# Kernel tuning notes

Hardware: AMD Instinct MI355X
Metric: run time of the kernel (lower is better)

The kernel has to match this reference:

```python
import jax, jax.numpy as jnp
import numpy as np

N_WIN = 232
T = 8
KERNEL = (2, 2, 2)
STRIDE = (2, 2, 2)
SLOPE = 25.0  # fast_sigmoid surrogate slope


@jax.custom_vjp
def spike(v):
    # heaviside(v) with fast-sigmoid surrogate gradient
    return (v > 0).astype(v.dtype)

def _spike_fwd(v):
    return spike(v), v

def _spike_bwd(v, g):
    return (g / (SLOPE * jnp.abs(v) + 1.0) ** 2,)

spike.defvjp(_spike_fwd, _spike_bwd)


def _avg_pool3d(x, kernel, stride):
    # x: (B, C, D, H, W), VALID pooling
    win = (1, 1) + tuple(kernel)
    st = (1, 1) + tuple(stride)
    s = jax.lax.reduce_window(x, 0.0, jax.lax.add, win, st, 'VALID')
    return s / float(np.prod(kernel))


def setup_inputs() -> dict:
    key = jax.random.key(0)
    ks = jax.random.split(key, 14)
    B, C, H, W = 64, 3, 32, 32
    input_dim, h0, h1, n_cls = 256, 256, 128, 6
    x = jax.random.normal(ks[0], (B, C, N_WIN, H, W), jnp.float32)
    W_in = jax.random.normal(ks[1], (h0, input_dim), jnp.float32) * 0.05
    b_in = jnp.zeros((h0,), jnp.float32)
    W_hid = jax.random.normal(ks[2], (h1, h0), jnp.float32) * 0.05
    b_hid = jnp.zeros((h1,), jnp.float32)
    in_feat = C * h1 * 14  # C * hidden[1] * D'
    W_out = jax.random.normal(ks[3], (n_cls, in_feat), jnp.float32) * 0.05
    b_out = jnp.zeros((n_cls,), jnp.float32)
    beta_in = jax.random.uniform(ks[4], (h0,), jnp.float32)
    thr_in = jax.random.uniform(ks[5], (h0,), jnp.float32)
    beta_hid = jax.random.uniform(ks[6], (h1,), jnp.float32)
    thr_hid = jax.random.uniform(ks[7], (h1,), jnp.float32)
    beta_out = jax.random.uniform(ks[8], (n_cls,), jnp.float32)
    return dict(x=x, W_in=W_in, b_in=b_in, W_hid=W_hid, b_hid=b_hid,
                W_out=W_out, b_out=b_out, beta_in=beta_in, thr_in=thr_in,
                beta_hid=beta_hid, thr_hid=thr_hid, beta_out=beta_out)


def _lif(mem, cur, beta, thr):
    # snntorch Leaky, reset-by-subtract; reset uses detached prev-mem spike
    reset = jax.lax.stop_gradient((mem > thr).astype(mem.dtype))
    mem = jnp.clip(beta, 0.0, 1.0) * mem + cur - reset * thr
    spk = spike(mem - thr)
    return spk, mem


def reference(x, W_in, b_in, W_hid, b_hid, W_out, b_out,
              beta_in, thr_in, beta_hid, thr_hid, beta_out):
    B, C, _, H, W = x.shape
    chunk = N_WIN // T  # 29
    # split depth into T chunks: (T, B, C, chunk, H, W)
    xt = x.reshape(B, C, T, chunk, H, W).transpose(2, 0, 1, 3, 4, 5)
    pooled = jax.vmap(lambda v: _avg_pool3d(v, KERNEL, STRIDE))(xt)  # (T,B,C,D',H',W')
    _, _, _, Dp, Hp, Wp = pooled.shape
    pr = pooled.reshape(T, B, C * Dp, Hp * Wp)
    # fc_in applied to all timesteps at once (recurrence-free)
    cur_in_all = jnp.einsum('tbnf,hf->tbnh', pr, W_in) + b_in  # (T,B,N,h0)

    h0 = W_in.shape[0]
    h1 = W_hid.shape[0]
    n_cls = W_out.shape[0]
    N = C * Dp
    mem_in0 = jnp.zeros((B, N, h0), x.dtype)
    mem_hid0 = jnp.zeros((B, N, h1), x.dtype)
    mem_out0 = jnp.zeros((B, n_cls), x.dtype)

    def step(carry, cur_in):
        mem_in, mem_hid, mem_out = carry
        spk_in, mem_in = _lif(mem_in, cur_in, beta_in, thr_in)
        cur_hid = jnp.einsum('bnh,gh->bng', spk_in, W_hid) + b_hid
        spk_hid, mem_hid = _lif(mem_hid, cur_hid, beta_hid, thr_hid)
        flat = spk_hid.reshape(spk_hid.shape[0], -1)  # (B, N*h1)
        cur_out = flat @ W_out.T + b_out
        spk_out, mem_out = _lif(mem_out, cur_out, beta_out, jnp.float32(1.0))
        return (mem_in, mem_hid, mem_out), spk_out

    _, spk_rec = jax.lax.scan(step, (mem_in0, mem_hid0, mem_out0), cur_in_all)
    return spk_rec  # (T, B, n_classes)
```

## Files before the change

kernel.cpp:

```cpp
#include <hip/hip_runtime.h>

#define T_STEPS 8
#define NROW    42
#define BN      2688
#define H0      256
#define H1      128
#define KFLAT   5376


#define SWA(r)  ((r) + ((r) >> 5) * 4)

__global__ __launch_bounds__(256, 3) void snn_front(
        const float* __restrict__ x,
        const float* __restrict__ Wi,
        const float* __restrict__ bi,
        const float* __restrict__ beti,
        const float* __restrict__ thri,
        const float* __restrict__ Wh,
        const float* __restrict__ bh,
        const float* __restrict__ beth,
        const float* __restrict__ thrh,
        float* __restrict__ spkh) {
    __shared__ float smem[9216 + 2240];
    float* S   = smem;
    float* At  = smem;
    float* Bt  = smem + 576;
    float* Bt2 = smem + 9216;

    int tid = threadIdx.x;
    int gbase = blockIdx.x * 4;

    int wp = tid & 15;
    int q  = tid >> 4;
    const float* xb0;
    const float* xb1;
    int mloc0 = q * 2, mloc1 = q * 2 + 1;
    {
        int g = gbase + (mloc0 >> 3);
        int t = mloc0 & 7;
        int b = g / 42, r = g - b * 42;
        int c = r / 14, dp = r - c * 14;
        xb0 = x + ((long)b * 712704 + (long)c * 237568
                + (long)(t * 29 + 2 * dp) * 1024 + 2 * wp);
    }
    {
        int g = gbase + (mloc1 >> 3);
        int t = mloc1 & 7;
        int b = g / 42, r = g - b * 42;
        int c = r / 14, dp = r - c * 14;
        xb1 = x + ((long)b * 712704 + (long)c * 237568
                + (long)(t * 29 + 2 * dp) * 1024 + 2 * wp);
    }

    const float* Bp = Wi + (long)tid * 256;
    int bcol = SWA(tid);

    int tm = tid & 3;
    int tn = tid >> 2;
    int ca = tm * 8;
    int cb = SWA(tn * 4);

    float acc[8][4] = {};

    for (int k0 = 0; k0 < 256; k0 += 16) {
        int hp = k0 >> 4;
        const float* p0 = xb0 + hp * 64;
        const float* p1 = xb1 + hp * 64;
        float2 a00 = *(const float2*)(p0);
        float2 a01 = *(const float2*)(p0 + 32);
        float2 a02 = *(const float2*)(p0 + 1024);
        float2 a03 = *(const float2*)(p0 + 1056);
        float2 a10 = *(const float2*)(p1);
        float2 a11 = *(const float2*)(p1 + 32);
        float2 a12 = *(const float2*)(p1 + 1024);
        float2 a13 = *(const float2*)(p1 + 1056);
        float4 w0 = *(const float4*)(Bp + k0);
        float4 w1 = *(const float4*)(Bp + k0 + 4);
        float4 w2 = *(const float4*)(Bp + k0 + 8);
        float4 w3 = *(const float4*)(Bp + k0 + 12);
        __syncthreads();
        float s0 = a00.x + a00.y + a01.x + a01.y + a02.x + a02.y + a03.x + a03.y;
        float s1 = a10.x + a10.y + a11.x + a11.y + a12.x + a12.y + a13.x + a13.y;
        At[wp * 36 + mloc0] = s0 * 0.125f;
        At[wp * 36 + mloc1] = s1 * 0.125f;
        Bt[ 0 * 284 + bcol] = w0.x; Bt[ 1 * 284 + bcol] = w0.y;
        Bt[ 2 * 284 + bcol] = w0.z; Bt[ 3 * 284 + bcol] = w0.w;
        Bt[ 4 * 284 + bcol] = w1.x; Bt[ 5 * 284 + bcol] = w1.y;
        Bt[ 6 * 284 + bcol] = w1.z; Bt[ 7 * 284 + bcol] = w1.w;
        Bt[ 8 * 284 + bcol] = w2.x; Bt[ 9 * 284 + bcol] = w2.y;
        Bt[10 * 284 + bcol] = w2.z; Bt[11 * 284 + bcol] = w2.w;
        Bt[12 * 284 + bcol] = w3.x; Bt[13 * 284 + bcol] = w3.y;
        Bt[14 * 284 + bcol] = w3.z; Bt[15 * 284 + bcol] = w3.w;
        __syncthreads();
#pragma unroll
        for (int k = 0; k < 16; ++k) {
            float4 av0 = *(const float4*)&At[k * 36 + ca];
            float4 av1 = *(const float4*)&At[k * 36 + ca + 4];
            float4 bv  = *(const float4*)&Bt[k * 284 + cb];
            float am[8] = {av0.x, av0.y, av0.z, av0.w, av1.x, av1.y, av1.z, av1.w};
            float bb[4] = {bv.x, bv.y, bv.z, bv.w};
#pragma unroll
            for (int i = 0; i < 8; ++i)
#pragma unroll
                for (int j = 0; j < 4; ++j)
                    acc[i][j] = fmaf(am[i], bb[j], acc[i][j]);
        }
    }

#pragma unroll
    for (int j = 0; j < 4; ++j) {
        int h = tn * 4 + j;
        float be = fminf(fmaxf(beti[h], 0.f), 1.f);
        float th = thri[h];
        float bb = bi[h];
        float mem = 0.f;
#pragma unroll
        for (int t = 0; t < T_STEPS; ++t) {
            float cur = acc[t][j] + bb;
            float reset = (mem > th) ? th : 0.f;
            mem = be * mem + cur - reset;
            acc[t][j] = ((mem - th) > 0.f) ? 1.f : 0.f;
        }
    }

    __syncthreads();
#pragma unroll
    for (int j = 0; j < 4; ++j) {
        int h = tn * 4 + j;
#pragma unroll
        for (int t = 0; t < T_STEPS; ++t)
            S[h * 36 + ca + t] = acc[t][j];
    }

    const float* Bp2 = Wh + (long)(tid >> 1) * 256 + (tid & 1) * 8;
    int bcol2 = SWA(tid >> 1);
    int cb2 = SWA(tn * 2);
    float acc2[8][2] = {};

    for (int k0 = 0; k0 < 256; k0 += 16) {
        float4 u0 = *(const float4*)(Bp2 + k0);
        float4 u1 = *(const float4*)(Bp2 + k0 + 4);
        __syncthreads();
        int kb = (tid & 1) * 8;
        Bt2[(kb + 0) * 140 + bcol2] = u0.x; Bt2[(kb + 1) * 140 + bcol2] = u0.y;
        Bt2[(kb + 2) * 140 + bcol2] = u0.z; Bt2[(kb + 3) * 140 + bcol2] = u0.w;
        Bt2[(kb + 4) * 140 + bcol2] = u1.x; Bt2[(kb + 5) * 140 + bcol2] = u1.y;
        Bt2[(kb + 6) * 140 + bcol2] = u1.z; Bt2[(kb + 7) * 140 + bcol2] = u1.w;
        __syncthreads();
#pragma unroll
        for (int k = 0; k < 16; ++k) {
            float4 av0 = *(const float4*)&S[(k0 + k) * 36 + ca];
            float4 av1 = *(const float4*)&S[(k0 + k) * 36 + ca + 4];
            float2 bv  = *(const float2*)&Bt2[k * 140 + cb2];
            float am[8] = {av0.x, av0.y, av0.z, av0.w, av1.x, av1.y, av1.z, av1.w};
#pragma unroll
            for (int i = 0; i < 8; ++i) {
                acc2[i][0] = fmaf(am[i], bv.x, acc2[i][0]);
                acc2[i][1] = fmaf(am[i], bv.y, acc2[i][1]);
            }
        }
    }

#pragma unroll
    for (int j = 0; j < 2; ++j) {
        int h = tn * 2 + j;
        float be = fminf(fmaxf(beth[h], 0.f), 1.f);
        float th = thrh[h];
        float bb = bh[h];
        float mem = 0.f;
#pragma unroll
        for (int t = 0; t < T_STEPS; ++t) {
            float cur = acc2[t][j] + bb;
            float reset = (mem > th) ? th : 0.f;
            mem = be * mem + cur - reset;
            acc2[t][j] = ((mem - th) > 0.f) ? 1.f : 0.f;
        }
    }
    int rbase = blockIdx.x * 32 + tm * 8;
#pragma unroll
    for (int t = 0; t < T_STEPS; ++t) {
        float2 o = {acc2[t][0], acc2[t][1]};
        *(float2*)&spkh[(long)(rbase + t) * 128 + tn * 2] = o;
    }
}

__global__ __launch_bounds__(256) void out_gemm(const float* __restrict__ spkh,
                                                const float* __restrict__ W_out,
                                                const float* __restrict__ b_out,
                                                float* __restrict__ cur_out) {
    __shared__ float part[256][8];
    int row = blockIdx.x;
    int t = row >> 6, b = row & 63;
    int tid = threadIdx.x;
    float acc[6] = {0.f, 0.f, 0.f, 0.f, 0.f, 0.f};
    for (int j = tid; j < KFLAT; j += 256) {
        int n = j >> 7, h = j & 127;
        float s = spkh[((long)(b * NROW + n) * 8 + t) * 128 + h];
#pragma unroll
        for (int c = 0; c < 6; ++c)
            acc[c] = fmaf(s, W_out[c * KFLAT + j], acc[c]);
    }
#pragma unroll
    for (int c = 0; c < 6; ++c) part[tid][c] = acc[c];
    __syncthreads();
    for (int off = 128; off > 0; off >>= 1) {
        if (tid < off) {
#pragma unroll
            for (int c = 0; c < 6; ++c) part[tid][c] += part[tid + off][c];
        }
        __syncthreads();
    }
    if (tid < 6) cur_out[row * 6 + tid] = part[0][tid] + b_out[tid];
}

__global__ void lif_out_kernel(const float* __restrict__ cur_out,
                               const float* __restrict__ beta_out,
                               float* __restrict__ out) {
    int j = threadIdx.x;
    if (j >= 384) return;
    int cls = j % 6;
    float be = fminf(fmaxf(beta_out[cls], 0.f), 1.f);
    float mem = 0.f;
#pragma unroll
    for (int t = 0; t < T_STEPS; ++t) {
        float cur = cur_out[t * 384 + j];
        float reset = (mem > 1.f) ? 1.f : 0.f;
        mem = be * mem + cur - reset;
        out[t * 384 + j] = ((mem - 1.f) > 0.f) ? 1.f : 0.f;
    }
}

extern "C" void kernel_launch(void* const* d_in, const int* in_sizes, int n_in,
                              void* d_out, int out_size, void* d_ws, size_t ws_size,
                              hipStream_t stream) {
    (void)in_sizes; (void)n_in; (void)out_size; (void)ws_size;
    const float* x        = (const float*)d_in[0];
    const float* W_in     = (const float*)d_in[1];
    const float* b_in     = (const float*)d_in[2];
    const float* W_hid    = (const float*)d_in[3];
    const float* b_hid    = (const float*)d_in[4];
    const float* W_out    = (const float*)d_in[5];
    const float* b_out    = (const float*)d_in[6];
    const float* beta_in  = (const float*)d_in[7];
    const float* thr_in   = (const float*)d_in[8];
    const float* beta_hid = (const float*)d_in[9];
    const float* thr_hid  = (const float*)d_in[10];
    const float* beta_out = (const float*)d_in[11];
    float* out = (float*)d_out;

    float* buf0 = (float*)d_ws;
    float* curo = buf0 + 2752512;

    snn_front<<<672, 256, 0, stream>>>(x, W_in, b_in, beta_in, thr_in,
                                       W_hid, b_hid, beta_hid, thr_hid, buf0);
    out_gemm<<<512, 256, 0, stream>>>(buf0, W_out, b_out, curo);
    lif_out_kernel<<<1, 384, 0, stream>>>(curo, beta_out, out);
}
```

Baseline: 342.5 us.

## Bit-pack hidden spikes, read W_hid from global, fuse output GEMM with LIF

In the front kernel, each thread packs its input-layer spike train for the 8 timesteps into one byte. The second GEMM now reads those bits from a small shared buffer and pulls W_hid rows straight from global memory instead of staging them through shared memory. This removes two barriers per k-step and most of the shared-memory footprint, which lets the occupancy hint rise to 4 blocks. The output GEMM and the output LIF are merged into one kernel with one 512-thread block per batch element, which drops a launch and an intermediate buffer. In exchange, that stage runs on only 64 blocks, and the inner loop gains bit-extract and convert instructions.

```diff
diff --git a/kernel.cpp b/kernel.cpp
--- a/kernel.cpp
+++ b/kernel.cpp
@@ -10,7 +10,7 @@
 
 #define SWA(r)  ((r) + ((r) >> 5) * 4)
 
-__global__ __launch_bounds__(256, 3) void snn_front(
+__global__ __launch_bounds__(256, 4) void snn_front(
         const float* __restrict__ x,
         const float* __restrict__ Wi,
         const float* __restrict__ bi,
@@ -21,11 +21,9 @@
         const float* __restrict__ beth,
         const float* __restrict__ thrh,
         float* __restrict__ spkh) {
-    __shared__ float smem[9216 + 2240];
-    float* S   = smem;
-    float* At  = smem;
-    float* Bt  = smem + 576;
-    float* Bt2 = smem + 9216;
+    __shared__ float At[16 * 36];
+    __shared__ float Bt[16 * 284];
+    __shared__ unsigned int S32[256];
 
     int tid = threadIdx.x;
     int gbase = blockIdx.x * 4;
@@ -107,6 +105,7 @@
         }
     }
 
+    unsigned int mybyte[4];
 #pragma unroll
     for (int j = 0; j < 4; ++j) {
         int h = tn * 4 + j;
@@ -114,49 +113,50 @@
         float th = thri[h];
         float bb = bi[h];
         float mem = 0.f;
+        unsigned int byte = 0u;
 #pragma unroll
         for (int t = 0; t < T_STEPS; ++t) {
             float cur = acc[t][j] + bb;
             float reset = (mem > th) ? th : 0.f;
             mem = be * mem + cur - reset;
-            acc[t][j] = ((mem - th) > 0.f) ? 1.f : 0.f;
-        }
-    }
-
+            byte |= ((mem - th) > 0.f) ? (1u << t) : 0u;
+        }
+        mybyte[j] = byte;
+    }
+    {
+        unsigned char* S8 = (unsigned char*)S32;
+#pragma unroll
+        for (int j = 0; j < 4; ++j)
+            S8[(tn * 4 + j) * 4 + tm] = (unsigned char)mybyte[j];
+    }
     __syncthreads();
-#pragma unroll
-    for (int j = 0; j < 4; ++j) {
-        int h = tn * 4 + j;
-#pragma unroll
-        for (int t = 0; t < T_STEPS; ++t)
-            S[h * 36 + ca + t] = acc[t][j];
-    }
-
-    const float* Bp2 = Wh + (long)(tid >> 1) * 256 + (tid & 1) * 8;
-    int bcol2 = SWA(tid >> 1);
-    int cb2 = SWA(tn * 2);
+
+    const float* wrow0 = Wh + (long)(tn * 2) * 256;
+    const float* wrow1 = wrow0 + 256;
+    int shift = tm * 8;
     float acc2[8][2] = {};
 
     for (int k0 = 0; k0 < 256; k0 += 16) {
-        float4 u0 = *(const float4*)(Bp2 + k0);
-        float4 u1 = *(const float4*)(Bp2 + k0 + 4);
-        __syncthreads();
-        int kb = (tid & 1) * 8;
-        Bt2[(kb + 0) * 140 + bcol2] = u0.x; Bt2[(kb + 1) * 140 + bcol2] = u0.y;
-        Bt2[(kb + 2) * 140 + bcol2] = u0.z; Bt2[(kb + 3) * 140 + bcol2] = u0.w;
-        Bt2[(kb + 4) * 140 + bcol2] = u1.x; Bt2[(kb + 5) * 140 + bcol2] = u1.y;
-        Bt2[(kb + 6) * 140 + bcol2] = u1.z; Bt2[(kb + 7) * 140 + bcol2] = u1.w;
-        __syncthreads();
+        float4 w00 = *(const float4*)(wrow0 + k0);
+        float4 w01 = *(const float4*)(wrow0 + k0 + 4);
+        float4 w02 = *(const float4*)(wrow0 + k0 + 8);
+        float4 w03 = *(const float4*)(wrow0 + k0 + 12);
+        float4 w10 = *(const float4*)(wrow1 + k0);
+        float4 w11 = *(const float4*)(wrow1 + k0 + 4);
+        float4 w12 = *(const float4*)(wrow1 + k0 + 8);
+        float4 w13 = *(const float4*)(wrow1 + k0 + 12);
+        float w0a[16] = {w00.x, w00.y, w00.z, w00.w, w01.x, w01.y, w01.z, w01.w,
+                         w02.x, w02.y, w02.z, w02.w, w03.x, w03.y, w03.z, w03.w};
+        float w1a[16] = {w10.x, w10.y, w10.z, w10.w, w11.x, w11.y, w11.z, w11.w,
+                         w12.x, w12.y, w12.z, w12.w, w13.x, w13.y, w13.z, w13.w};
 #pragma unroll
         for (int k = 0; k < 16; ++k) {
-            float4 av0 = *(const float4*)&S[(k0 + k) * 36 + ca];
-            float4 av1 = *(const float4*)&S[(k0 + k) * 36 + ca + 4];
-            float2 bv  = *(const float2*)&Bt2[k * 140 + cb2];
-            float am[8] = {av0.x, av0.y, av0.z, av0.w, av1.x, av1.y, av1.z, av1.w};
+            unsigned int sw = S32[k0 + k];
 #pragma unroll
             for (int i = 0; i < 8; ++i) {
-                acc2[i][0] = fmaf(am[i], bv.x, acc2[i][0]);
-                acc2[i][1] = fmaf(am[i], bv.y, acc2[i][1]);
+                float am = (float)((sw >> (shift + i)) & 1u);
+                acc2[i][0] = fmaf(am, w0a[k], acc2[i][0]);
+                acc2[i][1] = fmaf(am, w1a[k], acc2[i][1]);
             }
         }
     }
@@ -184,49 +184,53 @@
     }
 }
 
-__global__ __launch_bounds__(256) void out_gemm(const float* __restrict__ spkh,
-                                                const float* __restrict__ W_out,
-                                                const float* __restrict__ b_out,
-                                                float* __restrict__ cur_out) {
-    __shared__ float part[256][8];
-    int row = blockIdx.x;
-    int t = row >> 6, b = row & 63;
-    int tid = threadIdx.x;
-    float acc[6] = {0.f, 0.f, 0.f, 0.f, 0.f, 0.f};
-    for (int j = tid; j < KFLAT; j += 256) {
-        int n = j >> 7, h = j & 127;
-        float s = spkh[((long)(b * NROW + n) * 8 + t) * 128 + h];
-#pragma unroll
-        for (int c = 0; c < 6; ++c)
-            acc[c] = fmaf(s, W_out[c * KFLAT + j], acc[c]);
-    }
-#pragma unroll
-    for (int c = 0; c < 6; ++c) part[tid][c] = acc[c];
-    __syncthreads();
-    for (int off = 128; off > 0; off >>= 1) {
-        if (tid < off) {
-#pragma unroll
-            for (int c = 0; c < 6; ++c) part[tid][c] += part[tid + off][c];
-        }
-        __syncthreads();
-    }
-    if (tid < 6) cur_out[row * 6 + tid] = part[0][tid] + b_out[tid];
-}
-
-__global__ void lif_out_kernel(const float* __restrict__ cur_out,
-                               const float* __restrict__ beta_out,
-                               float* __restrict__ out) {
-    int j = threadIdx.x;
-    if (j >= 384) return;
-    int cls = j % 6;
-    float be = fminf(fmaxf(beta_out[cls], 0.f), 1.f);
-    float mem = 0.f;
-#pragma unroll
-    for (int t = 0; t < T_STEPS; ++t) {
-        float cur = cur_out[t * 384 + j];
-        float reset = (mem > 1.f) ? 1.f : 0.f;
-        mem = be * mem + cur - reset;
-        out[t * 384 + j] = ((mem - 1.f) > 0.f) ? 1.f : 0.f;
+__global__ __launch_bounds__(512) void out_fused(const float* __restrict__ spkh,
+                                                 const float* __restrict__ W_out,
+                                                 const float* __restrict__ b_out,
+                                                 const float* __restrict__ beta_out,
+                                                 float* __restrict__ out) {
+    __shared__ float part[2][256][8];
+    __shared__ float curs[8][8];
+    int b = blockIdx.x;
+    int grp = threadIdx.x >> 8;
+    int tid = threadIdx.x & 255;
+
+    for (int tr = 0; tr < 4; ++tr) {
+        int t = tr * 2 + grp;
+        float acc[6] = {0.f, 0.f, 0.f, 0.f, 0.f, 0.f};
+        for (int j = tid; j < KFLAT; j += 256) {
+            int n = j >> 7, h = j & 127;
+            float s = spkh[((long)(b * NROW + n) * 8 + t) * 128 + h];
+#pragma unroll
+            for (int c = 0; c < 6; ++c)
+                acc[c] = fmaf(s, W_out[c * KFLAT + j], acc[c]);
+        }
+#pragma unroll
+        for (int c = 0; c < 6; ++c) part[grp][tid][c] = acc[c];
+        __syncthreads();
+        for (int off = 128; off > 0; off >>= 1) {
+            if (tid < off) {
+#pragma unroll
+                for (int c = 0; c < 6; ++c)
+                    part[grp][tid][c] += part[grp][tid + off][c];
+            }
+            __syncthreads();
+        }
+        if (tid < 6) curs[t][tid] = part[grp][0][tid] + b_out[tid];
+        __syncthreads();
+    }
+
+    if (threadIdx.x < 6) {
+        int cls = threadIdx.x;
+        float be = fminf(fmaxf(beta_out[cls], 0.f), 1.f);
+        float mem = 0.f;
+#pragma unroll
+        for (int t = 0; t < T_STEPS; ++t) {
+            float cur = curs[t][cls];
+            float reset = (mem > 1.f) ? 1.f : 0.f;
+            mem = be * mem + cur - reset;
+            out[t * 384 + b * 6 + cls] = ((mem - 1.f) > 0.f) ? 1.f : 0.f;
+        }
     }
 }
 
@@ -249,10 +253,8 @@
     float* out = (float*)d_out;
 
     float* buf0 = (float*)d_ws;
-    float* curo = buf0 + 2752512;
 
     snn_front<<<672, 256, 0, stream>>>(x, W_in, b_in, beta_in, thr_in,
                                        W_hid, b_hid, beta_hid, thr_hid, buf0);
-    out_gemm<<<512, 256, 0, stream>>>(buf0, W_out, b_out, curo);
-    lif_out_kernel<<<1, 384, 0, stream>>>(curo, beta_out, out);
+    out_fused<<<64, 512, 0, stream>>>(buf0, W_out, b_out, beta_out, out);
 }
```

After: 370.8 us. +8.3%, slower.

## Widen front kernel to 512 threads and bit-pack input-layer spikes

Applied to the files above, without the earlier changes.

The fused front kernel now runs 512 threads per block, so each thread handles half the pooled rows and half the weight columns (8x2 tile instead of 8x4) in the first GEMM. Input-layer spikes are packed as 8-bit masks into a small shared array instead of a float matrix. The hidden GEMM now reads each thread's W_hid row straight from global memory with no shared staging or barriers, and multiplies by spike bits pulled out of the masks. Shared memory use drops sharply, but each thread reloads its full weight row, and the bit extraction plus int-to-float conversion adds ALU work.

```diff
diff --git a/kernel.cpp b/kernel.cpp
--- a/kernel.cpp
+++ b/kernel.cpp
@@ -10,7 +10,7 @@
 
 #define SWA(r)  ((r) + ((r) >> 5) * 4)
 
-__global__ __launch_bounds__(256, 3) void snn_front(
+__global__ __launch_bounds__(512) void snn_front(
         const float* __restrict__ x,
         const float* __restrict__ Wi,
         const float* __restrict__ bi,
@@ -21,167 +21,128 @@
         const float* __restrict__ beth,
         const float* __restrict__ thrh,
         float* __restrict__ spkh) {
-    __shared__ float smem[9216 + 2240];
-    float* S   = smem;
-    float* At  = smem;
-    float* Bt  = smem + 576;
-    float* Bt2 = smem + 9216;
+    __shared__ float At[16 * 36];
+    __shared__ float Bt[16 * 284];
+    __shared__ unsigned int S32[256];
 
     int tid = threadIdx.x;
     int gbase = blockIdx.x * 4;
 
-    int wp = tid & 15;
-    int q  = tid >> 4;
-    const float* xb0;
-    const float* xb1;
-    int mloc0 = q * 2, mloc1 = q * 2 + 1;
+    int sk = tid & 15;
+    int sm = tid >> 4;
+    const float* xb;
     {
-        int g = gbase + (mloc0 >> 3);
-        int t = mloc0 & 7;
+        int g = gbase + (sm >> 3);
+        int t = sm & 7;
         int b = g / 42, r = g - b * 42;
         int c = r / 14, dp = r - c * 14;
-        xb0 = x + ((long)b * 712704 + (long)c * 237568
-                + (long)(t * 29 + 2 * dp) * 1024 + 2 * wp);
-    }
-    {
-        int g = gbase + (mloc1 >> 3);
-        int t = mloc1 & 7;
-        int b = g / 42, r = g - b * 42;
-        int c = r / 14, dp = r - c * 14;
-        xb1 = x + ((long)b * 712704 + (long)c * 237568
-                + (long)(t * 29 + 2 * dp) * 1024 + 2 * wp);
-    }
-
-    const float* Bp = Wi + (long)tid * 256;
-    int bcol = SWA(tid);
-
-    int tm = tid & 3;
-    int tn = tid >> 2;
+        xb = x + ((long)b * 712704 + (long)c * 237568
+                + (long)(t * 29 + 2 * dp) * 1024 + 2 * sk);
+    }
+
+    int brow = tid >> 1;
+    int bq   = tid & 1;
+    const float* Bp = Wi + (long)brow * 256 + bq * 8;
+    int bcol = SWA(brow);
+
+    int tm = tid >> 7;
+    int tn = tid & 127;
     int ca = tm * 8;
-    int cb = SWA(tn * 4);
-
-    float acc[8][4] = {};
+    int cb = SWA(tn * 2);
+
+    float acc[8][2] = {};
 
     for (int k0 = 0; k0 < 256; k0 += 16) {
         int hp = k0 >> 4;
-        const float* p0 = xb0 + hp * 64;
-        const float* p1 = xb1 + hp * 64;
-        float2 a00 = *(const float2*)(p0);
-        float2 a01 = *(const float2*)(p0 + 32);
-        float2 a02 = *(const float2*)(p0 + 1024);
-        float2 a03 = *(const float2*)(p0 + 1056);
-        float2 a10 = *(const float2*)(p1);
-        float2 a11 = *(const float2*)(p1 + 32);
-        float2 a12 = *(const float2*)(p1 + 1024);
-        float2 a13 = *(const float2*)(p1 + 1056);
+        const float* p = xb + hp * 64;
+        float2 a0 = *(const float2*)(p);
+        float2 a1 = *(const float2*)(p + 32);
+        float2 a2 = *(const float2*)(p + 1024);
+        float2 a3 = *(const float2*)(p + 1056);
         float4 w0 = *(const float4*)(Bp + k0);
         float4 w1 = *(const float4*)(Bp + k0 + 4);
-        float4 w2 = *(const float4*)(Bp + k0 + 8);
-        float4 w3 = *(const float4*)(Bp + k0 + 12);
         __syncthreads();
-        float s0 = a00.x + a00.y + a01.x + a01.y + a02.x + a02.y + a03.x + a03.y;
-        float s1 = a10.x + a10.y + a11.x + a11.y + a12.x + a12.y + a13.x + a13.y;
-        At[wp * 36 + mloc0] = s0 * 0.125f;
-        At[wp * 36 + mloc1] = s1 * 0.125f;
-        Bt[ 0 * 284 + bcol] = w0.x; Bt[ 1 * 284 + bcol] = w0.y;
-        Bt[ 2 * 284 + bcol] = w0.z; Bt[ 3 * 284 + bcol] = w0.w;
-        Bt[ 4 * 284 + bcol] = w1.x; Bt[ 5 * 284 + bcol] = w1.y;
-        Bt[ 6 * 284 + bcol] = w1.z; Bt[ 7 * 284 + bcol] = w1.w;
-        Bt[ 8 * 284 + bcol] = w2.x; Bt[ 9 * 284 + bcol] = w2.y;
-        Bt[10 * 284 + bcol] = w2.z; Bt[11 * 284 + bcol] = w2.w;
-        Bt[12 * 284 + bcol] = w3.x; Bt[13 * 284 + bcol] = w3.y;
-        Bt[14 * 284 + bcol] = w3.z; Bt[15 * 284 + bcol] = w3.w;
+        float s0 = a0.x + a0.y + a1.x + a1.y + a2.x + a2.y + a3.x + a3.y;
+        At[sk * 36 + sm] = s0 * 0.125f;
+        int kb = bq * 8;
+        Bt[(kb + 0) * 284 + bcol] = w0.x; Bt[(kb + 1) * 284 + bcol] = w0.y;
+        Bt[(kb + 2) * 284 + bcol] = w0.z; Bt[(kb + 3) * 284 + bcol] = w0.w;
+        Bt[(kb + 4) * 284 + bcol] = w1.x; Bt[(kb + 5) * 284 + bcol] = w1.y;
+        Bt[(kb + 6) * 284 + bcol] = w1.z; Bt[(kb + 7) * 284 + bcol] = w1.w;
         __syncthreads();
 #pragma unroll
         for (int k = 0; k < 16; ++k) {
             float4 av0 = *(const float4*)&At[k * 36 + ca];
             float4 av1 = *(const float4*)&At[k * 36 + ca + 4];
-            float4 bv  = *(const float4*)&Bt[k * 284 + cb];
+            float2 bv  = *(const float2*)&Bt[k * 284 + cb];
             float am[8] = {av0.x, av0.y, av0.z, av0.w, av1.x, av1.y, av1.z, av1.w};
-            float bb[4] = {bv.x, bv.y, bv.z, bv.w};
-#pragma unroll
-            for (int i = 0; i < 8; ++i)
-#pragma unroll
-                for (int j = 0; j < 4; ++j)
-                    acc[i][j] = fmaf(am[i], bb[j], acc[i][j]);
-        }
-    }
-
-#pragma unroll
-    for (int j = 0; j < 4; ++j) {
-        int h = tn * 4 + j;
+#pragma unroll
+            for (int i = 0; i < 8; ++i) {
+                acc[i][0] = fmaf(am[i], bv.x, acc[i][0]);
+                acc[i][1] = fmaf(am[i], bv.y, acc[i][1]);
+            }
+        }
+    }
+
+#pragma unroll
+    for (int j = 0; j < 2; ++j) {
+        int h = tn * 2 + j;
         float be = fminf(fmaxf(beti[h], 0.f), 1.f);
         float th = thri[h];
         float bb = bi[h];
         float mem = 0.f;
+        unsigned int byte = 0u;
 #pragma unroll
         for (int t = 0; t < T_STEPS; ++t) {
             float cur = acc[t][j] + bb;
             float reset = (mem > th) ? th : 0.f;
             mem = be * mem + cur - reset;
-            acc[t][j] = ((mem - th) > 0.f) ? 1.f : 0.f;
-        }
-    }
-
+            byte |= ((mem - th) > 0.f) ? (1u << t) : 0u;
+        }
+        ((unsigned char*)S32)[h * 4 + tm] = (unsigned char)byte;
+    }
     __syncthreads();
-#pragma unroll
-    for (int j = 0; j < 4; ++j) {
-        int h = tn * 4 + j;
-#pragma unroll
-        for (int t = 0; t < T_STEPS; ++t)
-            S[h * 36 + ca + t] = acc[t][j];
-    }
-
-    const float* Bp2 = Wh + (long)(tid >> 1) * 256 + (tid & 1) * 8;
-    int bcol2 = SWA(tid >> 1);
-    int cb2 = SWA(tn * 2);
-    float acc2[8][2] = {};
+
+    const float* wrow = Wh + (long)tn * 256;
+    int shift = tm * 8;
+    float acc2[8] = {};
 
     for (int k0 = 0; k0 < 256; k0 += 16) {
-        float4 u0 = *(const float4*)(Bp2 + k0);
-        float4 u1 = *(const float4*)(Bp2 + k0 + 4);
-        __syncthreads();
-        int kb = (tid & 1) * 8;
-        Bt2[(kb + 0) * 140 + bcol2] = u0.x; Bt2[(kb + 1) * 140 + bcol2] = u0.y;
-        Bt2[(kb + 2) * 140 + bcol2] = u0.z; Bt2[(kb + 3) * 140 + bcol2] = u0.w;
-        Bt2[(kb + 4) * 140 + bcol2] = u1.x; Bt2[(kb + 5) * 140 + bcol2] = u1.y;
-        Bt2[(kb + 6) * 140 + bcol2] = u1.z; Bt2[(kb + 7) * 140 + bcol2] = u1.w;
-        __syncthreads();
+        float4 u0 = *(const float4*)(wrow + k0);
+        float4 u1 = *(const float4*)(wrow + k0 + 4);
+        float4 u2 = *(const float4*)(wrow + k0 + 8);
+        float4 u3 = *(const float4*)(wrow + k0 + 12);
+        float wa[16] = {u0.x, u0.y, u0.z, u0.w, u1.x, u1.y, u1.z, u1.w,
+                        u2.x, u2.y, u2.z, u2.w, u3.x, u3.y, u3.z, u3.w};
 #pragma unroll
         for (int k = 0; k < 16; ++k) {
-            float4 av0 = *(const float4*)&S[(k0 + k) * 36 + ca];
-            float4 av1 = *(const float4*)&S[(k0 + k) * 36 + ca + 4];
-            float2 bv  = *(const float2*)&Bt2[k * 140 + cb2];
-            float am[8] = {av0.x, av0.y, av0.z, av0.w, av1.x, av1.y, av1.z, av1.w};
+            unsigned int sw = S32[k0 + k];
 #pragma unroll
             for (int i = 0; i < 8; ++i) {
-                acc2[i][0] = fmaf(am[i], bv.x, acc2[i][0]);
-                acc2[i][1] = fmaf(am[i], bv.y, acc2[i][1]);
+                float am = (float)((sw >> (shift + i)) & 1u);
+                acc2[i] = fmaf(am, wa[k], acc2[i]);
             }
         }
     }
 
-#pragma unroll
-    for (int j = 0; j < 2; ++j) {
-        int h = tn * 2 + j;
+    {
+        int h = tn;
         float be = fminf(fmaxf(beth[h], 0.f), 1.f);
         float th = thrh[h];
         float bb = bh[h];
         float mem = 0.f;
 #pragma unroll
         for (int t = 0; t < T_STEPS; ++t) {
-            float cur = acc2[t][j] + bb;
+            float cur = acc2[t] + bb;
             float reset = (mem > th) ? th : 0.f;
             mem = be * mem + cur - reset;
-            acc2[t][j] = ((mem - th) > 0.f) ? 1.f : 0.f;
+            acc2[t] = ((mem - th) > 0.f) ? 1.f : 0.f;
         }
     }
     int rbase = blockIdx.x * 32 + tm * 8;
 #pragma unroll
-    for (int t = 0; t < T_STEPS; ++t) {
-        float2 o = {acc2[t][0], acc2[t][1]};
-        *(float2*)&spkh[(long)(rbase + t) * 128 + tn * 2] = o;
-    }
+    for (int t = 0; t < T_STEPS; ++t)
+        spkh[(long)(rbase + t) * 128 + tn] = acc2[t];
 }
 
 __global__ __launch_bounds__(256) void out_gemm(const float* __restrict__ spkh,
@@ -251,7 +212,7 @@
     float* buf0 = (float*)d_ws;
     float* curo = buf0 + 2752512;
 
-    snn_front<<<672, 256, 0, stream>>>(x, W_in, b_in, beta_in, thr_in,
+    snn_front<<<672, 512, 0, stream>>>(x, W_in, b_in, beta_in, thr_in,
                                        W_hid, b_hid, beta_hid, thr_hid, buf0);
     out_gemm<<<512, 256, 0, stream>>>(buf0, W_out, b_out, curo);
     lif_out_kernel<<<1, 384, 0, stream>>>(curo, beta_out, out);
```

Result: slower. 389.6 us (+13.8%).
